# Performance work log

Measured on AMD Instinct MI355X. Metric: run time of the kernel, lower is better.

## Reference

```python
import jax, jax.numpy as jnp
import numpy as np

D, W, H = 128, 128, 128          # volume obj_shape (d, w, h)
RES_SCALE = 1.4
RES_D = int(D * RES_SCALE)       # 179 detector rows
RES_H = int(H * RES_SCALE)       # 179 detector cols
N_PROJ = 10


def setup_inputs() -> dict:
    key = jax.random.key(0)
    k1, k2 = jax.random.split(key, 2)
    # learnable reconstruction volume, initialized to ones (torch.ones_like)
    I_rec = jnp.ones((1, 1, D, W, H), dtype=jnp.float32)
    # emitter positions, scaled to volume size; y-component kept away from the
    # source plane y=0 so that ray directions are well-conditioned
    poses = jax.random.uniform(k1, (50, 3), dtype=jnp.float32)
    poses = poses * jnp.array([D, W, H], jnp.float32) + jnp.array([-64.0, 256.0, -64.0], jnp.float32)
    idx = jax.random.randint(k2, (N_PROJ,), 0, 50, dtype=jnp.int32)
    return {"I_rec": I_rec, "poses": poses, "idx": idx}


def _trilinear_3d(vol, coords):
    """torch F.grid_sample 3D, bilinear, align_corners=False, zero padding.
    vol: [D, Hd, Wd]; coords: [..., 3] in (x, y, z) normalized to [-1, 1],
    where x indexes the last (Wd) axis, y the middle, z the first."""
    Dv, Hv, Wv = vol.shape
    x, y, z = coords[..., 0], coords[..., 1], coords[..., 2]
    ix = ((x + 1.0) * Wv - 1.0) * 0.5
    iy = ((y + 1.0) * Hv - 1.0) * 0.5
    iz = ((z + 1.0) * Dv - 1.0) * 0.5
    x0f, y0f, z0f = jnp.floor(ix), jnp.floor(iy), jnp.floor(iz)
    tx, ty, tz = ix - x0f, iy - y0f, iz - z0f
    x0 = x0f.astype(jnp.int32); y0 = y0f.astype(jnp.int32); z0 = z0f.astype(jnp.int32)
    x1, y1, z1 = x0 + 1, y0 + 1, z0 + 1

    def gather(zc, yc, xc):
        valid = (zc >= 0) & (zc < Dv) & (yc >= 0) & (yc < Hv) & (xc >= 0) & (xc < Wv)
        v = vol[jnp.clip(zc, 0, Dv - 1), jnp.clip(yc, 0, Hv - 1), jnp.clip(xc, 0, Wv - 1)]
        return jnp.where(valid, v, 0.0)

    out = (
        gather(z0, y0, x0) * (1 - tz) * (1 - ty) * (1 - tx)
        + gather(z0, y0, x1) * (1 - tz) * (1 - ty) * tx
        + gather(z0, y1, x0) * (1 - tz) * ty * (1 - tx)
        + gather(z0, y1, x1) * (1 - tz) * ty * tx
        + gather(z1, y0, x0) * tz * (1 - ty) * (1 - tx)
        + gather(z1, y0, x1) * tz * (1 - ty) * tx
        + gather(z1, y1, x0) * tz * ty * (1 - tx)
        + gather(z1, y1, x1) * tz * ty * tx
    )
    return out


def _project_one(vol, emi):
    """vol: [D, W, H]; emi: [3] emitter position. Returns [RES_D, RES_H]."""
    lin_x = jnp.linspace(-RES_D / 2.0, RES_D / 2.0 - 1.0, RES_D, dtype=jnp.float32)
    lin_y = jnp.linspace(-RES_H / 2.0, RES_H / 2.0 - 1.0, RES_H, dtype=jnp.float32)
    gx, gy = jnp.meshgrid(lin_x, lin_y, indexing="ij")            # [Gx, Gy]
    rays = jnp.stack([gx, jnp.zeros_like(gx), gy], axis=-1) - emi  # [Gx, Gy, 3]
    rays = rays / jnp.linalg.norm(rays, axis=-1, keepdims=True)
    dx = jnp.abs(1.0 / rays[..., 1])                               # [Gx, Gy]
    # (P0 - I0) . N  with N = (0,1,0): source-plane y samples minus emitter y
    p0y = jnp.linspace(0.0, W - 1.0, W, dtype=jnp.float32)         # [K=W]
    T = (1.0 / rays[..., 1])[..., None] * (p0y - emi[1])           # [Gx, Gy, K]
    grid = rays[..., None, :] * T[..., None] + emi                 # [Gx, Gy, K, 3]
    g0 = grid[..., 0] / D * 2.0
    g1 = grid[..., 1] / W * 2.0 - 1.0
    g2 = grid[..., 2] / H * 2.0
    coords = jnp.stack([g2, g1, g0], axis=-1)  # torch.flip(grid, [3]) -> (x,y,z)
    samp = _trilinear_3d(vol, coords)          # [Gx, Gy, K]
    return jnp.sum(samp, axis=-1) * dx


def reference(I_rec, poses, idx):
    sel = poses[idx]  # [10, 3]
    vol = I_rec[0, 0]
    projections = jax.vmap(lambda e: _project_one(vol, e))(sel)  # [10, Gx, Gy]
    return projections[None], idx
```

## Files before the change

kernel.cpp:

```cpp
#include <hip/hip_runtime.h>
#include <hip/hip_bf16.h>
#include <stdint.h>


#define DVOL   128
#define RES    179
#define NPROJ  10
#define OUT_PROJ (NPROJ * RES * RES)
#define BATCH  8

#define IL_A   132
#define IL_C   130
#define IL_SLAB (IL_C * IL_A)
#define IL_TOT  (DVOL * IL_SLAB)

__device__ __forceinline__ uint32_t bfbits(float v) {
    __hip_bfloat16 h = __float2bfloat16(v);
    return (uint32_t)*(unsigned short*)&h;
}

__global__ __launch_bounds__(128) void pad_kernel(const float* __restrict__ vol,
                                                  uint32_t* __restrict__ il) {
    const int q = blockIdx.x;
    const int p = blockIdx.y;
    const int a = threadIdx.x;
    const int wlo = q * 17;
    const int whi = min(130, wlo + 17);
    uint32_t* slab = il + p * IL_SLAB;

    uint32_t prev = 0;
    {
        const int c = wlo - 1;
        if (c >= 0 && c < 128) {
            const float* src = vol + (c << 14) + (p << 7) + a;
            float v = src[0];
            if (p >= 1) v += src[-128];
            prev = bfbits(v);
        }
    }
    #pragma unroll 2
    for (int c = wlo; c < whi; ++c) {
        uint32_t cur = 0;
        if (c < 128) {
            const float* src = vol + (c << 14) + (p << 7) + a;
            float v = src[0];
            if (p >= 1) v += src[-128];
            cur = bfbits(v);
        }
        slab[c * IL_A + (a + 1)] = (cur << 16) | prev;
        prev = cur;
    }
    for (int b = a; b < (whi - wlo) * 4; b += 128) {
        const int w  = wlo + (b >> 2);
        const int bi = b & 3;
        const int ai = (bi == 0) ? 0 : (128 + bi);
        slab[w * IL_A + ai] = 0u;
    }
}

__device__ __forceinline__ void axis_interval(float base, float slope, float lo, float hi,
                                              float& t0, float& t1) {
    if (fabsf(slope) < 1e-9f) {
        const bool in = (base >= lo && base <= hi);
        t0 = in ? -1e30f : 1e30f;
        t1 = in ?  1e30f : -1e30f;
    } else {
        const float inv = 1.0f / slope;
        const float a = (lo - base) * inv;
        const float b = (hi - base) * inv;
        t0 = fminf(a, b);
        t1 = fmaxf(a, b);
    }
}

__device__ __forceinline__ int wave_imin(int v) {
    #pragma unroll
    for (int o = 32; o; o >>= 1) v = min(v, __shfl_xor(v, o, 64));
    return v;
}
__device__ __forceinline__ int wave_imax(int v) {
    #pragma unroll
    for (int o = 32; o; o >>= 1) v = max(v, __shfl_xor(v, o, 64));
    return v;
}

__device__ __forceinline__ float asf(uint32_t u) { return __uint_as_float(u); }

#define ISSUE(tc_, ta_, w_, b_) do {                                          \
    const int base_ = (b_) * BATCH;                                           \
    const float afb_ = fmaf((float)base_, sz, af0);                           \
    _Pragma("unroll")                                                         \
    for (int k = 0; k < BATCH; ++k) {                                         \
        const uint2 t = tab[wid][base_ + k];           \
        tc_[k] = asf(t.x);                                                    \
        const float af1 = __builtin_amdgcn_fmed3f(                            \
            fmaf((float)k, sz, afb_), 0.0f, 129.0f);                          \
        ta_[k] = __builtin_amdgcn_fractf(af1);                                \
        const uint32_t off = t.y + (uint32_t)(int)af1;     \
        w_[k] = *(const uint2*)(il + off);                                    \
    }                                                                         \
} while (0)

#define CONSUME(tc_, ta_, w_) do {                                            \
    _Pragma("unroll")                                                         \
    for (int k = 0; k < BATCH; ++k) {                                         \
        const float f00 = asf(w_[k].x << 16);          \
        const float f10 = asf(w_[k].x & 0xffff0000u);  \
        const float f01 = asf(w_[k].y << 16);          \
        const float f11 = asf(w_[k].y & 0xffff0000u);  \
        const float h0 = fmaf(ta_[k], f01 - f00, f00);                        \
        const float h1 = fmaf(ta_[k], f11 - f10, f10);                        \
        acc += fmaf(tc_[k], h1 - h0, h0);                                     \
    }                                                                         \
} while (0)

__global__ __launch_bounds__(128) void proj_fast(
    const uint32_t* __restrict__ il,
    const float* __restrict__ poses,
    const int* __restrict__ idx,
    float* __restrict__ out)
{
    __shared__ uint2 tab[2][DVOL];

    const int lane = threadIdx.x & 63;
    const int wid  = threadIdx.x >> 6;
    int gj = blockIdx.x * 64 + lane;
    int gi = blockIdx.y * 2 + wid;
    const int j = blockIdx.z;

    if (blockIdx.x == 0 && blockIdx.y == 0 && j == 0 && threadIdx.x < NPROJ)
        out[OUT_PROJ + threadIdx.x] = (float)idx[threadIdx.x];

    const bool store_ok = (gi < RES) && (gj < RES);
    gi = min(gi, RES - 1);
    gj = min(gj, RES - 1);

    const int pid = idx[j];
    const float ex = poses[pid * 3 + 0];
    const float ey = poses[pid * 3 + 1];
    const float ez = poses[pid * 3 + 2];

    const float pdx = (float)gi - 89.5f;
    const float pdz = (float)gj - 89.5f;

    const float inv_ey = 1.0f / ey;
    const float sx = (ex - pdx) * inv_ey;
    const float sz = (ez - pdz) * inv_ey;
    const float ddx = pdx - ex, ddz = pdz - ez;
    const float dxw = sqrtf(ddx * ddx + ey * ey + ddz * ddz) * fabsf(inv_ey);
    const float cb = pdx + 63.5f;
    const float ab = pdz + 63.5f;

    float gc0, gc1, ga0, ga1;
    axis_interval(cb, sx, -1.0f, 128.0f, gc0, gc1);
    axis_interval(ab, sz, -1.0f, 128.0f, ga0, ga1);
    const float q_lo = fmaxf(fmaxf(gc0, ga0), 0.0f);
    const float q_hi = fminf(fminf(gc1, ga1), 127.0f);
    int q0, q1;
    if (q_lo <= q_hi + 0.5f) {
        q0 = max(0, (int)ceilf(q_lo) - 1);
        q1 = min(DVOL, (int)floorf(q_hi) + 2);
    } else { q0 = DVOL; q1 = 0; }
    int Q0 = wave_imin(q0);
    int Q1 = wave_imax(q1);
    Q0 = __builtin_amdgcn_readfirstlane(Q0);
    Q1 = __builtin_amdgcn_readfirstlane(Q1);

    const int n = Q1 - Q0;
    for (int e = lane; e < n; e += 64) {
        const int p = Q0 + e;
        const float cf1 = __builtin_amdgcn_fmed3f(
            fmaf((float)p, sx, cb) + 1.0f, 0.0f, 129.0f);
        const int c0i = (int)cf1;
        uint2 t;
        t.x = __float_as_uint(__builtin_amdgcn_fractf(cf1));
        t.y = (uint32_t)(p * IL_SLAB + c0i * IL_A);
        tab[wid][e] = t;
    }

    float acc = 0.0f;
    const float af0 = fmaf((float)Q0, sz, ab + 1.0f);

    float tcA[BATCH], taA[BATCH]; uint2 wA[BATCH];
    float tcB[BATCH], taB[BATCH]; uint2 wB[BATCH];

    const int nb = (n > 0) ? (n >> 3) : 0;
    if (nb >= 2) {
        ISSUE(tcA, taA, wA, 0);
        int b = 0;
        for (; b + 2 < nb; b += 2) {
            ISSUE(tcB, taB, wB, b + 1);
            CONSUME(tcA, taA, wA);
            ISSUE(tcA, taA, wA, b + 2);
            CONSUME(tcB, taB, wB);
        }
        if (b + 1 < nb) {
            ISSUE(tcB, taB, wB, b + 1);
            CONSUME(tcA, taA, wA);
            CONSUME(tcB, taB, wB);
        } else {
            CONSUME(tcA, taA, wA);
        }
    } else if (nb == 1) {
        ISSUE(tcA, taA, wA, 0);
        CONSUME(tcA, taA, wA);
    }

    for (int pe = nb << 3; pe < n; ++pe) {
        const uint2 t = tab[wid][pe];
        const float tc = asf(t.x);
        const float af1 = __builtin_amdgcn_fmed3f(
            fmaf((float)pe, sz, af0), 0.0f, 129.0f);
        const float ta = __builtin_amdgcn_fractf(af1);
        const uint32_t off = t.y + (uint32_t)(int)af1;
        const uint2 w2 = *(const uint2*)(il + off);
        const float f00 = asf(w2.x << 16);
        const float f10 = asf(w2.x & 0xffff0000u);
        const float f01 = asf(w2.y << 16);
        const float f11 = asf(w2.y & 0xffff0000u);
        const float h0 = fmaf(ta, f01 - f00, f00);
        const float h1 = fmaf(ta, f11 - f10, f10);
        acc += fmaf(tc, h1 - h0, h0);
    }

    if (store_ok) out[j * (RES * RES) + gi * RES + gj] = acc * (0.5f * dxw);
}

__global__ __launch_bounds__(256) void proj_kernel_fb(
    const float* __restrict__ vol, const float* __restrict__ poses,
    const int* __restrict__ idx, float* __restrict__ out)
{
    const int gj = blockIdx.x * 64 + (threadIdx.x & 63);
    const int gi = blockIdx.y * 4 + (threadIdx.x >> 6);
    const int j  = blockIdx.z;
    if (blockIdx.x == 0 && blockIdx.y == 0 && j == 0 && threadIdx.x < NPROJ)
        out[OUT_PROJ + threadIdx.x] = (float)idx[threadIdx.x];
    if (gi >= RES || gj >= RES) return;
    const int pid = idx[j];
    const float ex = poses[pid*3+0], ey = poses[pid*3+1], ez = poses[pid*3+2];
    const float pdx = (float)gi - 89.5f, pdz = (float)gj - 89.5f;
    const float inv_ey = 1.0f / ey;
    const float sx = (ex - pdx) * inv_ey, sz = (ez - pdz) * inv_ey;
    const float ddx = pdx - ex, ddz = pdz - ez;
    const float dxw = sqrtf(ddx*ddx + ey*ey + ddz*ddz) * fabsf(inv_ey);
    const float cb = pdx + 63.5f, ab = pdz + 63.5f;
    float acc = 0.0f;
    for (int p = 0; p < DVOL; ++p) {
        const float cf = fmaf((float)p, sx, cb);
        const float af = fmaf((float)p, sz, ab);
        if (cf >= -1.0f && cf < 128.0f && af >= -1.0f && af < 128.0f) {
            const float c0f = floorf(cf), a0f = floorf(af);
            const float tc = cf - c0f, ta = af - a0f;
            const int c0 = (int)c0f, a0 = (int)a0f;
            const float wc0 = (c0 >= 0)   ? (1.0f - tc) : 0.0f;
            const float wc1 = (c0 <= 126) ? tc          : 0.0f;
            const float wa0 = (a0 >= 0)   ? (1.0f - ta) : 0.0f;
            const float wa1 = (a0 <= 126) ? ta          : 0.0f;
            const int c0c = c0 < 0 ? 0 : c0;
            const int c1c = c0 >= 127 ? 127 : c0 + 1;
            const int a0c = a0 < 0 ? 0 : a0;
            const int a1c = a0 >= 127 ? 127 : a0 + 1;
            const float w00 = wc0*wa0, w01 = wc0*wa1, w10 = wc1*wa0, w11 = wc1*wa1;
            const int b0 = (c0c << 14) + (p << 7);
            const int b1 = (c1c << 14) + (p << 7);
            float s = w00*vol[b0+a0c] + w01*vol[b0+a1c] + w10*vol[b1+a0c] + w11*vol[b1+a1c];
            if (p >= 1)
                s += w00*vol[b0+a0c-128] + w01*vol[b0+a1c-128]
                   + w10*vol[b1+a0c-128] + w11*vol[b1+a1c-128];
            acc += 0.5f * s;
        }
    }
    out[j * (RES * RES) + gi * RES + gj] = acc * dxw;
}

extern "C" void kernel_launch(void* const* d_in, const int* in_sizes, int n_in,
                              void* d_out, int out_size, void* d_ws, size_t ws_size,
                              hipStream_t stream) {
    const float* vol   = (const float*)d_in[0];
    const float* poses = (const float*)d_in[1];
    const int*   idx   = (const int*)d_in[2];
    float* out = (float*)d_out;

    if (ws_size >= (size_t)IL_TOT * sizeof(uint32_t)) {
        uint32_t* ilbuf = (uint32_t*)d_ws;
        dim3 pgrid(8, DVOL);
        pad_kernel<<<pgrid, 128, 0, stream>>>(vol, ilbuf);
        dim3 grid(3 , 90 , NPROJ);
        proj_fast<<<grid, 128, 0, stream>>>(ilbuf, poses, idx, out);
    } else {
        dim3 grid(3, 45, NPROJ);
        proj_kernel_fb<<<grid, 256, 0, stream>>>(vol, poses, idx, out);
    }
}
```

Measured before the change: 92.26 us.

## Store padded volume as plain bf16 grid and gather four 16-bit corners

The preprocessed volume changes from an interleaved layout, where each 32-bit word packs two neighbouring c-samples, to a plain bf16 array with one extra padded row. That halves the workspace footprint. Each sample now issues four 16-bit loads instead of one 64-bit load, and the pipelining batch shrinks from 8 to 6 to make room for the larger per-sample registers. The smaller footprint may improve cache hit rates, but the extra load instructions add issue overhead.

After: 107.4 us. 16.4% more time.

```diff
diff --git a/kernel.cpp b/kernel.cpp
--- a/kernel.cpp
+++ b/kernel.cpp
@@ -7,12 +7,14 @@
 #define RES    179
 #define NPROJ  10
 #define OUT_PROJ (NPROJ * RES * RES)
-#define BATCH  8
-
-#define IL_A   132
-#define IL_C   130
-#define IL_SLAB (IL_C * IL_A)
-#define IL_TOT  (DVOL * IL_SLAB)
+#define BATCH  6
+
+#define IL_AW   132
+#define IL_CR   131
+#define IL_ROWB (IL_AW * 2)
+#define IL_SLABW (IL_CR * IL_AW)
+#define IL_SLABB (IL_SLABW * 2)
+#define IL_TOTB  ((size_t)DVOL * IL_SLABB)
 
 __device__ __forceinline__ uint32_t bfbits(float v) {
     __hip_bfloat16 h = __float2bfloat16(v);
@@ -20,41 +22,30 @@
 }
 
 __global__ __launch_bounds__(128) void pad_kernel(const float* __restrict__ vol,
-                                                  uint32_t* __restrict__ il) {
+                                                  unsigned short* __restrict__ il16) {
     const int q = blockIdx.x;
     const int p = blockIdx.y;
     const int a = threadIdx.x;
     const int wlo = q * 17;
-    const int whi = min(130, wlo + 17);
-    uint32_t* slab = il + p * IL_SLAB;
-
-    uint32_t prev = 0;
-    {
-        const int c = wlo - 1;
+    const int whi = min(IL_CR, wlo + 17);
+    unsigned short* slab = il16 + p * IL_SLABW;
+
+    for (int ci = wlo; ci < whi; ++ci) {
+        const int c = ci - 1;
+        uint32_t b = 0;
         if (c >= 0 && c < 128) {
             const float* src = vol + (c << 14) + (p << 7) + a;
             float v = src[0];
             if (p >= 1) v += src[-128];
-            prev = bfbits(v);
-        }
-    }
-    #pragma unroll 2
-    for (int c = wlo; c < whi; ++c) {
-        uint32_t cur = 0;
-        if (c < 128) {
-            const float* src = vol + (c << 14) + (p << 7) + a;
-            float v = src[0];
-            if (p >= 1) v += src[-128];
-            cur = bfbits(v);
-        }
-        slab[c * IL_A + (a + 1)] = (cur << 16) | prev;
-        prev = cur;
-    }
-    for (int b = a; b < (whi - wlo) * 4; b += 128) {
-        const int w  = wlo + (b >> 2);
-        const int bi = b & 3;
+            b = bfbits(v);
+        }
+        slab[ci * IL_AW + (a + 1)] = (unsigned short)b;
+    }
+    for (int bidx = a; bidx < (whi - wlo) * 4; bidx += 128) {
+        const int w  = wlo + (bidx >> 2);
+        const int bi = bidx & 3;
         const int ai = (bi == 0) ? 0 : (128 + bi);
-        slab[w * IL_A + ai] = 0u;
+        slab[w * IL_AW + ai] = 0;
     }
 }
 
@@ -86,7 +77,7 @@
 
 __device__ __forceinline__ float asf(uint32_t u) { return __uint_as_float(u); }
 
-#define ISSUE(tc_, ta_, w_, b_) do {                                          \
+#define ISSUE(tc_, ta_, u_, b_) do {                                          \
     const int base_ = (b_) * BATCH;                                           \
     const float afb_ = fmaf((float)base_, sz, af0);                           \
     _Pragma("unroll")                                                         \
@@ -96,18 +87,21 @@
         const float af1 = __builtin_amdgcn_fmed3f(                            \
             fmaf((float)k, sz, afb_), 0.0f, 129.0f);                          \
         ta_[k] = __builtin_amdgcn_fractf(af1);                                \
-        const uint32_t off = t.y + (uint32_t)(int)af1;     \
-        w_[k] = *(const uint2*)(il + off);                                    \
+        const uint8_t* pb = il8 + t.y + (((uint32_t)(int)af1) << 1);          \
+        u_[k].x = *(const unsigned short*)(pb);               \
+        u_[k].y = *(const unsigned short*)(pb + 2);           \
+        u_[k].z = *(const unsigned short*)(pb + IL_ROWB);     \
+        u_[k].w = *(const unsigned short*)(pb + IL_ROWB + 2); \
     }                                                                         \
 } while (0)
 
-#define CONSUME(tc_, ta_, w_) do {                                            \
+#define CONSUME(tc_, ta_, u_) do {                                            \
     _Pragma("unroll")                                                         \
     for (int k = 0; k < BATCH; ++k) {                                         \
-        const float f00 = asf(w_[k].x << 16);          \
-        const float f10 = asf(w_[k].x & 0xffff0000u);  \
-        const float f01 = asf(w_[k].y << 16);          \
-        const float f11 = asf(w_[k].y & 0xffff0000u);  \
+        const float f00 = asf(u_[k].x << 16);                                 \
+        const float f01 = asf(u_[k].y << 16);                                 \
+        const float f10 = asf(u_[k].z << 16);                                 \
+        const float f11 = asf(u_[k].w << 16);                                 \
         const float h0 = fmaf(ta_[k], f01 - f00, f00);                        \
         const float h1 = fmaf(ta_[k], f11 - f10, f10);                        \
         acc += fmaf(tc_[k], h1 - h0, h0);                                     \
@@ -115,7 +109,7 @@
 } while (0)
 
 __global__ __launch_bounds__(128) void proj_fast(
-    const uint32_t* __restrict__ il,
+    const uint8_t* __restrict__ il8,
     const float* __restrict__ poses,
     const int* __restrict__ idx,
     float* __restrict__ out)
@@ -174,50 +168,53 @@
         const int c0i = (int)cf1;
         uint2 t;
         t.x = __float_as_uint(__builtin_amdgcn_fractf(cf1));
-        t.y = (uint32_t)(p * IL_SLAB + c0i * IL_A);
+        t.y = (uint32_t)(p * IL_SLABB + c0i * IL_ROWB);
         tab[wid][e] = t;
     }
 
     float acc = 0.0f;
     const float af0 = fmaf((float)Q0, sz, ab + 1.0f);
 
-    float tcA[BATCH], taA[BATCH]; uint2 wA[BATCH];
-    float tcB[BATCH], taB[BATCH]; uint2 wB[BATCH];
-
-    const int nb = (n > 0) ? (n >> 3) : 0;
+    float tcA[BATCH], taA[BATCH]; uint4 uA[BATCH];
+    float tcB[BATCH], taB[BATCH]; uint4 uB[BATCH];
+
+    const int nb = (n > 0) ? (n / BATCH) : 0;
     if (nb >= 2) {
-        ISSUE(tcA, taA, wA, 0);
+        ISSUE(tcA, taA, uA, 0);
         int b = 0;
         for (; b + 2 < nb; b += 2) {
-            ISSUE(tcB, taB, wB, b + 1);
-            CONSUME(tcA, taA, wA);
-            ISSUE(tcA, taA, wA, b + 2);
-            CONSUME(tcB, taB, wB);
+            ISSUE(tcB, taB, uB, b + 1);
+            CONSUME(tcA, taA, uA);
+            ISSUE(tcA, taA, uA, b + 2);
+            CONSUME(tcB, taB, uB);
         }
         if (b + 1 < nb) {
-            ISSUE(tcB, taB, wB, b + 1);
-            CONSUME(tcA, taA, wA);
-            CONSUME(tcB, taB, wB);
+            ISSUE(tcB, taB, uB, b + 1);
+            CONSUME(tcA, taA, uA);
+            CONSUME(tcB, taB, uB);
         } else {
-            CONSUME(tcA, taA, wA);
+            CONSUME(tcA, taA, uA);
         }
     } else if (nb == 1) {
-        ISSUE(tcA, taA, wA, 0);
-        CONSUME(tcA, taA, wA);
-    }
-
-    for (int pe = nb << 3; pe < n; ++pe) {
+        ISSUE(tcA, taA, uA, 0);
+        CONSUME(tcA, taA, uA);
+    }
+
+    for (int pe = nb * BATCH; pe < n; ++pe) {
         const uint2 t = tab[wid][pe];
         const float tc = asf(t.x);
         const float af1 = __builtin_amdgcn_fmed3f(
             fmaf((float)pe, sz, af0), 0.0f, 129.0f);
         const float ta = __builtin_amdgcn_fractf(af1);
-        const uint32_t off = t.y + (uint32_t)(int)af1;
-        const uint2 w2 = *(const uint2*)(il + off);
-        const float f00 = asf(w2.x << 16);
-        const float f10 = asf(w2.x & 0xffff0000u);
-        const float f01 = asf(w2.y << 16);
-        const float f11 = asf(w2.y & 0xffff0000u);
+        const uint8_t* pb = il8 + t.y + (((uint32_t)(int)af1) << 1);
+        const uint32_t u00 = *(const unsigned short*)(pb);
+        const uint32_t u01 = *(const unsigned short*)(pb + 2);
+        const uint32_t u10 = *(const unsigned short*)(pb + IL_ROWB);
+        const uint32_t u11 = *(const unsigned short*)(pb + IL_ROWB + 2);
+        const float f00 = asf(u00 << 16);
+        const float f01 = asf(u01 << 16);
+        const float f10 = asf(u10 << 16);
+        const float f11 = asf(u11 << 16);
         const float h0 = fmaf(ta, f01 - f00, f00);
         const float h1 = fmaf(ta, f11 - f10, f10);
         acc += fmaf(tc, h1 - h0, h0);
@@ -281,12 +278,12 @@
     const int*   idx   = (const int*)d_in[2];
     float* out = (float*)d_out;
 
-    if (ws_size >= (size_t)IL_TOT * sizeof(uint32_t)) {
-        uint32_t* ilbuf = (uint32_t*)d_ws;
+    if (ws_size >= IL_TOTB) {
+        unsigned short* ilbuf = (unsigned short*)d_ws;
         dim3 pgrid(8, DVOL);
         pad_kernel<<<pgrid, 128, 0, stream>>>(vol, ilbuf);
         dim3 grid(3 , 90 , NPROJ);
-        proj_fast<<<grid, 128, 0, stream>>>(ilbuf, poses, idx, out);
+        proj_fast<<<grid, 128, 0, stream>>>((const uint8_t*)ilbuf, poses, idx, out);
     } else {
         dim3 grid(3, 45, NPROJ);
         proj_kernel_fb<<<grid, 256, 0, stream>>>(vol, poses, idx, out);
```

## Deepen gather prefetch to triple buffering and recompute fractions in consume

Applied to the files above, without the earlier changes.

The sample loop moves from a two-stage to a three-stage software pipeline, so two batches of volume gathers are in flight while a third is consumed. The fractional z weights are no longer held in registers between issue and consume; they are recomputed inside CONSUME to save registers. The extra in-flight buffer raises register pressure and may cut occupancy, and recomputing the fractions adds ALU work.

Result: slower. 96.34 us (+4.4%).

```diff
diff --git a/kernel.cpp b/kernel.cpp
--- a/kernel.cpp
+++ b/kernel.cpp
@@ -86,7 +86,7 @@
 
 __device__ __forceinline__ float asf(uint32_t u) { return __uint_as_float(u); }
 
-#define ISSUE(tc_, ta_, w_, b_) do {                                          \
+#define ISSUE(tc_, w_, b_) do {                                               \
     const int base_ = (b_) * BATCH;                                           \
     const float afb_ = fmaf((float)base_, sz, af0);                           \
     _Pragma("unroll")                                                         \
@@ -95,21 +95,25 @@
         tc_[k] = asf(t.x);                                                    \
         const float af1 = __builtin_amdgcn_fmed3f(                            \
             fmaf((float)k, sz, afb_), 0.0f, 129.0f);                          \
-        ta_[k] = __builtin_amdgcn_fractf(af1);                                \
-        const uint32_t off = t.y + (uint32_t)(int)af1;     \
+        const uint32_t off = t.y + (uint32_t)(int)af1;                        \
         w_[k] = *(const uint2*)(il + off);                                    \
     }                                                                         \
 } while (0)
 
-#define CONSUME(tc_, ta_, w_) do {                                            \
+#define CONSUME(tc_, w_, b_) do {                                             \
+    const int base_ = (b_) * BATCH;                                           \
+    const float afb_ = fmaf((float)base_, sz, af0);                           \
     _Pragma("unroll")                                                         \
     for (int k = 0; k < BATCH; ++k) {                                         \
+        const float af1 = __builtin_amdgcn_fmed3f(                            \
+            fmaf((float)k, sz, afb_), 0.0f, 129.0f);                          \
+        const float ta = __builtin_amdgcn_fractf(af1);                        \
         const float f00 = asf(w_[k].x << 16);          \
         const float f10 = asf(w_[k].x & 0xffff0000u);  \
         const float f01 = asf(w_[k].y << 16);          \
         const float f11 = asf(w_[k].y & 0xffff0000u);  \
-        const float h0 = fmaf(ta_[k], f01 - f00, f00);                        \
-        const float h1 = fmaf(ta_[k], f11 - f10, f10);                        \
+        const float h0 = fmaf(ta, f01 - f00, f00);                            \
+        const float h1 = fmaf(ta, f11 - f10, f10);                            \
         acc += fmaf(tc_[k], h1 - h0, h0);                                     \
     }                                                                         \
 } while (0)
@@ -181,29 +185,38 @@
     float acc = 0.0f;
     const float af0 = fmaf((float)Q0, sz, ab + 1.0f);
 
-    float tcA[BATCH], taA[BATCH]; uint2 wA[BATCH];
-    float tcB[BATCH], taB[BATCH]; uint2 wB[BATCH];
+    float tcA[BATCH]; uint2 wA[BATCH];
+    float tcB[BATCH]; uint2 wB[BATCH];
+    float tcC[BATCH]; uint2 wC[BATCH];
 
     const int nb = (n > 0) ? (n >> 3) : 0;
     if (nb >= 2) {
-        ISSUE(tcA, taA, wA, 0);
+        ISSUE(tcA, wA, 0);
+        ISSUE(tcB, wB, 1);
         int b = 0;
-        for (; b + 2 < nb; b += 2) {
-            ISSUE(tcB, taB, wB, b + 1);
-            CONSUME(tcA, taA, wA);
-            ISSUE(tcA, taA, wA, b + 2);
-            CONSUME(tcB, taB, wB);
-        }
-        if (b + 1 < nb) {
-            ISSUE(tcB, taB, wB, b + 1);
-            CONSUME(tcA, taA, wA);
-            CONSUME(tcB, taB, wB);
+        for (; b + 4 < nb; b += 3) {
+            ISSUE(tcC, wC, b + 2);  CONSUME(tcA, wA, b);
+            ISSUE(tcA, wA, b + 3);  CONSUME(tcB, wB, b + 1);
+            ISSUE(tcB, wB, b + 4);  CONSUME(tcC, wC, b + 2);
+        }
+        const int rem = nb - b;
+        if (rem == 2) {
+            CONSUME(tcA, wA, b);
+            CONSUME(tcB, wB, b + 1);
+        } else if (rem == 3) {
+            ISSUE(tcC, wC, b + 2);
+            CONSUME(tcA, wA, b);
+            CONSUME(tcB, wB, b + 1);
+            CONSUME(tcC, wC, b + 2);
         } else {
-            CONSUME(tcA, taA, wA);
+            ISSUE(tcC, wC, b + 2);  CONSUME(tcA, wA, b);
+            ISSUE(tcA, wA, b + 3);  CONSUME(tcB, wB, b + 1);
+            CONSUME(tcC, wC, b + 2);
+            CONSUME(tcA, wA, b + 3);
         }
     } else if (nb == 1) {
-        ISSUE(tcA, taA, wA, 0);
-        CONSUME(tcA, taA, wA);
+        ISSUE(tcA, wA, 0);
+        CONSUME(tcA, wA, 0);
     }
 
     for (int pe = nb << 3; pe < n; ++pe) {
```
